# Kernel tuning notes

Measured on AMD Instinct MI355X. Metric: run time of the kernel, lower is better.

## Reference

```python
import jax, jax.numpy as jnp
import numpy as np

N = 100000   # node_num / batch_node_num (full-graph batch, identity remap)
E = 600000   # edges in adj[nodes, :]
D_IN = 128
D_OUT = 128
MASK = (1.0, 1.0, 0.0, 0.0)  # self-loop mask per `ind` in original forward


def setup_inputs() -> dict:
    key = jax.random.key(0)
    ks = jax.random.split(key, 6)
    feat = jax.random.normal(ks[0], (N, D_IN), dtype=jnp.float32)
    edge_src = jax.random.randint(ks[1], (E,), 0, N)
    edge_dst = jax.random.randint(ks[2], (E,), 0, N)
    W_edge = jax.random.uniform(ks[3], (E,), dtype=jnp.float32)  # W[u][v] per edge
    W1 = jax.random.normal(ks[4], (D_IN, D_OUT), dtype=jnp.float32) / np.sqrt(D_IN).astype(np.float32)
    b1 = jnp.zeros((D_OUT,), jnp.float32)
    W2 = jax.random.normal(ks[5], (D_OUT, D_OUT), dtype=jnp.float32) / np.sqrt(D_OUT).astype(np.float32)
    b2 = jnp.zeros((D_OUT,), jnp.float32)
    return {"feat": feat, "W_edge": W_edge, "W1": W1, "b1": b1, "W2": W2,
            "b2": b2, "edge_src": edge_src, "edge_dst": edge_dst, "ind": 2}


def reference(feat, W_edge, W1, b1, W2, b2, edge_src, edge_dst, ind):
    # values: self-loop edges get mask[ind], others 1 (torch.where on edges[:,0]==edges[:,1])
    mask_val = MASK[ind]  # ind is a static Python int
    values = jnp.where(edge_src == edge_dst, jnp.float32(mask_val), jnp.float32(1.0))
    # degree[v] = row-sum of matrix_coo (spmm with ones); temp_e = degree[dst_e]
    degree = jax.ops.segment_sum(values, edge_src, num_segments=N)
    # new_embeddings = Linear -> Tanh -> Linear on features of (all) unique nodes
    h = jnp.tanh(feat @ W1 + b1) @ W2 + b2  # [N, D_OUT]
    # matrix = matrix_neighbor .* matrix_weight -> per-edge weight degree[dst]*W[u][v]
    w = degree[edge_dst] * W_edge  # [E]
    # results = spmm(matrix, new_embeddings); row_sum = spmm(matrix, ones)
    results = jax.ops.segment_sum(w[:, None] * h[edge_dst], edge_src, num_segments=N)
    row_sum = jax.ops.segment_sum(w, edge_src, num_segments=N)
    row_sum = jnp.where(row_sum == 0, jnp.float32(1.0), row_sum)
    return results / row_sum[:, None]
```

## Files before the change

### kernel.cpp

```cpp
#include <hip/hip_runtime.h>


constexpr int D = 128;
constexpr int MAXDEG = 24;
constexpr int OVF_CAP = 131072;

typedef __attribute__((ext_vector_type(8))) short short8;
typedef __attribute__((ext_vector_type(4))) float f32x4;
struct ushort8_s { unsigned short v[8]; };

__device__ __forceinline__ unsigned short f2bf(float x) {
    unsigned int u = __float_as_uint(x);
    u += 0x7fffu + ((u >> 16) & 1u);
    return (unsigned short)(u >> 16);
}
__device__ __forceinline__ float bflo(unsigned int u) { return __uint_as_float(u << 16); }
__device__ __forceinline__ float bfhi(unsigned int u) { return __uint_as_float(u & 0xffff0000u); }
__device__ __forceinline__ float fast_tanh(float x) {
    float e = exp2f(x * 2.885390081777927f);
    return fmaf(-2.0f, __builtin_amdgcn_rcpf(e + 1.0f), 1.0f);
}
__device__ __forceinline__ int swz(int row, int kbyte) {
    return (row * 256 + kbyte) ^ ((row & 7) << 4);
}

__global__ __launch_bounds__(256) void k_init(const float* __restrict__ W1,
                                              const float* __restrict__ W2,
                                              unsigned short* __restrict__ Wt1s,
                                              unsigned short* __restrict__ Wt2s,
                                              int* __restrict__ zbase, int zv4) {
    int b = blockIdx.x;
    if (b < 64) {
        int t = b * 256 + threadIdx.x;
        int k = t >> 7, nn = t & 127;
        int si = swz(nn, k * 2) >> 1;
        Wt1s[si] = f2bf(W1[t]);
        Wt2s[si] = f2bf(W2[t]);
    } else {
        int i = (b - 64) * 256 + threadIdx.x;
        if (i < zv4) ((int4*)zbase)[i] = make_int4(0, 0, 0, 0);
    }
}

__global__ __launch_bounds__(512, 4) void k_mlp_place(
        const float* __restrict__ feat,
        const unsigned short* __restrict__ Wt1s,
        const unsigned short* __restrict__ Wt2s,
        const float* __restrict__ b1, const float* __restrict__ b2,
        unsigned short* __restrict__ hbf, int n,
        const int* __restrict__ src, const int* __restrict__ dst,
        const float* __restrict__ W_edge,
        unsigned int* __restrict__ packed,
        int* __restrict__ ovf_cnt, int4* __restrict__ ovf,
        float2* __restrict__ pairs, int E, int epb) {
    __shared__ unsigned short sW1[128 * D];
    __shared__ unsigned short sW2[128 * D];
    const int t = threadIdx.x;
    const int lane = t & 63;
    const int w = t >> 6;
    const int rl0 = w * 16;
    const int row0 = blockIdx.x * 128 + rl0;
    const int rA = lane & 15;
    const int ks = (lane >> 4) * 8;

    const int ebase = blockIdx.x * epb;
    const int e1 = ebase + t;
    const int e2 = e1 + 512;
    const bool v1 = (t < epb) && (e1 < E);
    const bool v2 = (t < epb - 512) && (e2 < E);
    int s1 = 0, d1 = 0, s2 = 0, d2 = 0;
    float ew1 = 0.f, ew2 = 0.f;
    if (v1) { s1 = src[e1]; d1 = dst[e1]; ew1 = W_edge[e1]; }
    if (v2) { s2 = src[e2]; d2 = dst[e2]; ew2 = W_edge[e2]; }

    float4 f[4][2];
    {
        int gr = row0 + rA;
        bool ok = gr < n;
        const float* fp = &feat[(size_t)(ok ? gr : 0) * D + ks];
#pragma unroll
        for (int kc = 0; kc < 4; ++kc) {
            f[kc][0] = ok ? *(const float4*)(fp + kc * 32) : make_float4(0.f, 0.f, 0.f, 0.f);
            f[kc][1] = ok ? *(const float4*)(fp + kc * 32 + 4) : make_float4(0.f, 0.f, 0.f, 0.f);
        }
    }

    {
        const ushort8_s* g1 = (const ushort8_s*)Wt1s;
        const ushort8_s* g2 = (const ushort8_s*)Wt2s;
        ushort8_s* l1 = (ushort8_s*)sW1;
        ushort8_s* l2 = (ushort8_s*)sW2;
#pragma unroll
        for (int j = 0; j < 4; ++j) {
            int c = t + j * 512;
            l1[c] = g1[c];
            l2[c] = g2[c];
        }
    }

    unsigned int old1 = 0, old2 = 0;
    if (v1) old1 = atomicAdd(&packed[s1], (s1 == d1) ? 0x10001u : 1u);
    if (v2) old2 = atomicAdd(&packed[s2], (s2 == d2) ? 0x10001u : 1u);

    float bias1[8], bias2[8];
#pragma unroll
    for (int nf = 0; nf < 8; ++nf) {
        bias1[nf] = b1[nf * 16 + rA];
        bias2[nf] = b2[nf * 16 + rA];
    }

    short8 afrag[4];
#pragma unroll
    for (int kc = 0; kc < 4; ++kc) {
        float4 f0 = f[kc][0], f1 = f[kc][1];
        short8 a;
        a[0] = (short)f2bf(f0.x); a[1] = (short)f2bf(f0.y);
        a[2] = (short)f2bf(f0.z); a[3] = (short)f2bf(f0.w);
        a[4] = (short)f2bf(f1.x); a[5] = (short)f2bf(f1.y);
        a[6] = (short)f2bf(f1.z); a[7] = (short)f2bf(f1.w);
        afrag[kc] = a;
    }

    __syncthreads();

    f32x4 acc[8];
#pragma unroll
    for (int nf = 0; nf < 8; ++nf) acc[nf] = (f32x4){0.f, 0.f, 0.f, 0.f};

#pragma unroll
    for (int kc = 0; kc < 4; ++kc) {
        const int kb = (kc * 32 + ks) * 2;
#pragma unroll
        for (int nf = 0; nf < 8; ++nf) {
            const int rb = nf * 16 + rA;
            short8 b = *(short8*)((char*)sW1 + swz(rb, kb));
            acc[nf] = __builtin_amdgcn_mfma_f32_16x16x32_bf16(afrag[kc], b, acc[nf], 0, 0, 0);
        }
    }

    __syncthreads();

#pragma unroll
    for (int nf = 0; nf < 8; ++nf) {
        const int col = nf * 16 + rA;
#pragma unroll
        for (int i = 0; i < 4; ++i) {
            const int rl = rl0 + (lane >> 4) * 4 + i;
            unsigned short hv = f2bf(fast_tanh(acc[nf][i] + bias1[nf]));
            *(unsigned short*)((char*)sW1 + swz(rl, col * 2)) = hv;
        }
    }

#pragma unroll
    for (int nf = 0; nf < 8; ++nf) acc[nf] = (f32x4){0.f, 0.f, 0.f, 0.f};

#pragma unroll
    for (int kc = 0; kc < 4; ++kc) {
        const int kb = (kc * 32 + ks) * 2;
        const int ra0 = rl0 + rA;
        short8 a0 = *(short8*)((char*)sW1 + swz(ra0, kb));
#pragma unroll
        for (int nf = 0; nf < 8; ++nf) {
            const int rb = nf * 16 + rA;
            short8 b = *(short8*)((char*)sW2 + swz(rb, kb));
            acc[nf] = __builtin_amdgcn_mfma_f32_16x16x32_bf16(a0, b, acc[nf], 0, 0, 0);
        }
    }

#pragma unroll
    for (int nf = 0; nf < 8; ++nf) {
        const int col = nf * 16 + rA;
#pragma unroll
        for (int i = 0; i < 4; ++i) {
            const int rl = rl0 + (lane >> 4) * 4 + i;
            unsigned short hv = f2bf(acc[nf][i] + bias2[nf]);
            *(unsigned short*)((char*)sW1 + swz(rl, col * 2)) = hv;
        }
    }

    for (int c = lane; c < 256; c += 64) {
        int r = c >> 4, k0 = (c & 15) * 8;
        int gr = row0 + r;
        if (gr < n) {
            int rl = rl0 + r;
            short8 v = *(short8*)((char*)sW1 + swz(rl, k0 * 2));
            *(short8*)&hbf[(size_t)gr * D + k0] = v;
        }
    }

    if (v1) {
        int rank = (int)(old1 & 0xffffu);
        if (rank < MAXDEG) {
            unsigned long long pk =
                (unsigned long long)(unsigned int)d1 |
                ((unsigned long long)__float_as_uint(ew1) << 32);
            __builtin_nontemporal_store(pk, (unsigned long long*)&pairs[(size_t)s1 * MAXDEG + rank]);
        } else {
            int oi = atomicAdd(ovf_cnt, 1);
            if (oi < OVF_CAP) ovf[oi] = make_int4(s1, d1, __float_as_int(ew1), 0);
        }
    }
    if (v2) {
        int rank = (int)(old2 & 0xffffu);
        if (rank < MAXDEG) {
            unsigned long long pk =
                (unsigned long long)(unsigned int)d2 |
                ((unsigned long long)__float_as_uint(ew2) << 32);
            __builtin_nontemporal_store(pk, (unsigned long long*)&pairs[(size_t)s2 * MAXDEG + rank]);
        } else {
            int oi = atomicAdd(ovf_cnt, 1);
            if (oi < OVF_CAP) ovf[oi] = make_int4(s2, d2, __float_as_int(ew2), 0);
        }
    }
}

__global__ __launch_bounds__(256) void k_aggregate(const unsigned int* __restrict__ packed,
                                                   const float2* __restrict__ pairs,
                                                   const int* __restrict__ ovf_cnt,
                                                   const int4* __restrict__ ovf,
                                                   const unsigned short* __restrict__ hbf,
                                                   const int* __restrict__ indp,
                                                   float* __restrict__ out, int n) {
    long long tid = (long long)blockIdx.x * 256 + threadIdx.x;
    int node = (int)(tid >> 4);
    int li = (int)(tid & 15);
    int lane = threadIdx.x & 63;
    if (node >= n) return;
    const float maskm1 = ((indp[0] < 2) ? 1.0f : 0.0f) - 1.0f;

    int cnt = (int)(packed[node] & 0xffffu);
    int mt = (cnt < MAXDEG) ? cnt : MAXDEG;

    float acc[8];
#pragma unroll
    for (int j = 0; j < 8; ++j) acc[j] = 0.f;
    float rsp = 0.f;
    const int gbase = lane & 48;
    const float2* prow = &pairs[(size_t)node * MAXDEG];

    auto fma8 = [&](float w, uint4 h) {
        acc[0] = fmaf(w, bflo(h.x), acc[0]); acc[1] = fmaf(w, bfhi(h.x), acc[1]);
        acc[2] = fmaf(w, bflo(h.y), acc[2]); acc[3] = fmaf(w, bfhi(h.y), acc[3]);
        acc[4] = fmaf(w, bflo(h.z), acc[4]); acc[5] = fmaf(w, bfhi(h.z), acc[5]);
        acc[6] = fmaf(w, bflo(h.w), acc[6]); acc[7] = fmaf(w, bfhi(h.w), acc[7]);
    };

    for (int base = 0; base < mt; base += 16) {
        int mm = mt - base;
        mm = (mm > 16) ? 16 : mm;
        float wv = 0.f;
        float dv = 0.f;
        if (li < mm) {
            float2 p = prow[base + li];
            dv = p.x;
            int d = __float_as_int(p.x);
            unsigned int pkd = packed[d];
            float deg = (float)(pkd & 0xffffu) + maskm1 * (float)(pkd >> 16);
            wv = deg * p.y;
        }
        rsp += wv;
        int i = 0;
        for (; i + 3 < mm; i += 4) {
            int d0 = __float_as_int(__shfl(dv, gbase + i));
            float w0 = __shfl(wv, gbase + i);
            int d1 = __float_as_int(__shfl(dv, gbase + i + 1));
            float w1 = __shfl(wv, gbase + i + 1);
            int d2 = __float_as_int(__shfl(dv, gbase + i + 2));
            float w2 = __shfl(wv, gbase + i + 2);
            int d3 = __float_as_int(__shfl(dv, gbase + i + 3));
            float w3 = __shfl(wv, gbase + i + 3);
            uint4 h0 = *(const uint4*)&hbf[(size_t)d0 * D + li * 8];
            uint4 h1 = *(const uint4*)&hbf[(size_t)d1 * D + li * 8];
            uint4 h2 = *(const uint4*)&hbf[(size_t)d2 * D + li * 8];
            uint4 h3 = *(const uint4*)&hbf[(size_t)d3 * D + li * 8];
            fma8(w0, h0); fma8(w1, h1); fma8(w2, h2); fma8(w3, h3);
        }
        for (; i + 1 < mm; i += 2) {
            int d0 = __float_as_int(__shfl(dv, gbase + i));
            float w0 = __shfl(wv, gbase + i);
            int d1 = __float_as_int(__shfl(dv, gbase + i + 1));
            float w1 = __shfl(wv, gbase + i + 1);
            uint4 h0 = *(const uint4*)&hbf[(size_t)d0 * D + li * 8];
            uint4 h1 = *(const uint4*)&hbf[(size_t)d1 * D + li * 8];
            fma8(w0, h0); fma8(w1, h1);
        }
        if (i < mm) {
            int d0 = __float_as_int(__shfl(dv, gbase + i));
            float w0 = __shfl(wv, gbase + i);
            uint4 h0 = *(const uint4*)&hbf[(size_t)d0 * D + li * 8];
            fma8(w0, h0);
        }
    }

    int ovn = *ovf_cnt;
    if (ovn > OVF_CAP) ovn = OVF_CAP;
    for (int i = 0; i < ovn; ++i) {
        int4 tq = ovf[i];
        if (tq.x == node) {
            int d = tq.y;
            unsigned int pkd = packed[d];
            float deg = (float)(pkd & 0xffffu) + maskm1 * (float)(pkd >> 16);
            float w = deg * __int_as_float(tq.z);
            if (li == 0) rsp += w;
            uint4 h = *(const uint4*)&hbf[(size_t)d * D + li * 8];
            fma8(w, h);
        }
    }

    rsp += __shfl_xor(rsp, 1);
    rsp += __shfl_xor(rsp, 2);
    rsp += __shfl_xor(rsp, 4);
    rsp += __shfl_xor(rsp, 8);
    rsp = (rsp == 0.f) ? 1.f : rsp;
    float inv = 1.0f / rsp;
    float4 o0, o1;
    o0.x = acc[0] * inv; o0.y = acc[1] * inv; o0.z = acc[2] * inv; o0.w = acc[3] * inv;
    o1.x = acc[4] * inv; o1.y = acc[5] * inv; o1.z = acc[6] * inv; o1.w = acc[7] * inv;
    float* op = &out[(size_t)node * D + li * 8];
    *(float4*)op = o0;
    *(float4*)(op + 4) = o1;
}

extern "C" void kernel_launch(void* const* d_in, const int* in_sizes, int n_in,
                              void* d_out, int out_size, void* d_ws, size_t ws_size,
                              hipStream_t stream) {
    const float* feat   = (const float*)d_in[0];
    const float* W_edge = (const float*)d_in[1];
    const float* W1     = (const float*)d_in[2];
    const float* b1     = (const float*)d_in[3];
    const float* W2     = (const float*)d_in[4];
    const float* b2     = (const float*)d_in[5];
    const int* edge_src = (const int*)d_in[6];
    const int* edge_dst = (const int*)d_in[7];
    const int* indp     = (const int*)d_in[8];

    const int n = in_sizes[0] / D;
    const int E = in_sizes[6];

    char* ws = (char*)d_ws;
    unsigned short* Wt1s = (unsigned short*)ws;
    unsigned short* Wt2s = Wt1s + D * D;
    unsigned int* packed = (unsigned int*)(Wt2s + D * D);
    int* ovf_cnt         = (int*)(packed + n);
    int4* ovf            = (int4*)((char*)ovf_cnt + 16);
    float2* pairs        = (float2*)(ovf + OVF_CAP);
    unsigned short* hbf  = (unsigned short*)(pairs + (size_t)n * MAXDEG);

    const int zbytes = n * 4 + 16;
    const int zv4 = zbytes / 16;
    const int zb = (zv4 + 255) / 256;
    k_init<<<64 + zb, 256, 0, stream>>>(W1, W2, Wt1s, Wt2s, (int*)packed, zv4);

    const int nm = (n + 127) / 128;
    const int epb = (E + nm - 1) / nm;
    k_mlp_place<<<nm, 512, 0, stream>>>(feat, Wt1s, Wt2s, b1, b2, hbf, n,
                                        edge_src, edge_dst, W_edge,
                                        packed, ovf_cnt, ovf, pairs, E, epb);

    long long athreads = (long long)n * 16;
    k_aggregate<<<(int)((athreads + 255) / 256), 256, 0, stream>>>(packed, pairs, ovf_cnt,
                                                                   ovf, hbf, indp,
                                                                   (float*)d_out, n);
}
```

Measured before the change: 98.47 us.

## Read second-layer weights from global memory instead of LDS, halving shared memory

The second MLP weight matrix is no longer staged into shared memory. It is stored transposed and unswizzled in global memory, and the B fragments are read directly from there (L1/L2 cached) during the second MFMA loop. This halves LDS use per block (64KB to 32KB), which could allow more resident blocks per CU and removes the W2 copy. The edge placement stores also switch from nontemporal to plain float2 stores, which changes how those writes interact with the cache before the aggregate kernel reads them. The cost is global-memory latency on the B-fragment loads inside the MFMA loop.

```diff
diff --git a/kernel.cpp b/kernel.cpp
--- a/kernel.cpp
+++ b/kernel.cpp
@@ -27,15 +27,14 @@
 __global__ __launch_bounds__(256) void k_init(const float* __restrict__ W1,
                                               const float* __restrict__ W2,
                                               unsigned short* __restrict__ Wt1s,
-                                              unsigned short* __restrict__ Wt2s,
+                                              unsigned short* __restrict__ Wt2t,
                                               int* __restrict__ zbase, int zv4) {
     int b = blockIdx.x;
     if (b < 64) {
         int t = b * 256 + threadIdx.x;
         int k = t >> 7, nn = t & 127;
-        int si = swz(nn, k * 2) >> 1;
-        Wt1s[si] = f2bf(W1[t]);
-        Wt2s[si] = f2bf(W2[t]);
+        Wt1s[swz(nn, k * 2) >> 1] = f2bf(W1[t]);
+        Wt2t[nn * D + k] = f2bf(W2[t]);
     } else {
         int i = (b - 64) * 256 + threadIdx.x;
         if (i < zv4) ((int4*)zbase)[i] = make_int4(0, 0, 0, 0);
@@ -45,7 +44,7 @@
 __global__ __launch_bounds__(512, 4) void k_mlp_place(
         const float* __restrict__ feat,
         const unsigned short* __restrict__ Wt1s,
-        const unsigned short* __restrict__ Wt2s,
+        const unsigned short* __restrict__ Wt2t,
         const float* __restrict__ b1, const float* __restrict__ b2,
         unsigned short* __restrict__ hbf, int n,
         const int* __restrict__ src, const int* __restrict__ dst,
@@ -54,7 +53,6 @@
         int* __restrict__ ovf_cnt, int4* __restrict__ ovf,
         float2* __restrict__ pairs, int E, int epb) {
     __shared__ unsigned short sW1[128 * D];
-    __shared__ unsigned short sW2[128 * D];
     const int t = threadIdx.x;
     const int lane = t & 63;
     const int w = t >> 6;
@@ -87,14 +85,11 @@
 
     {
         const ushort8_s* g1 = (const ushort8_s*)Wt1s;
-        const ushort8_s* g2 = (const ushort8_s*)Wt2s;
         ushort8_s* l1 = (ushort8_s*)sW1;
-        ushort8_s* l2 = (ushort8_s*)sW2;
 #pragma unroll
         for (int j = 0; j < 4; ++j) {
             int c = t + j * 512;
             l1[c] = g1[c];
-            l2[c] = g2[c];
         }
     }
 
@@ -161,8 +156,7 @@
         short8 a0 = *(short8*)((char*)sW1 + swz(ra0, kb));
 #pragma unroll
         for (int nf = 0; nf < 8; ++nf) {
-            const int rb = nf * 16 + rA;
-            short8 b = *(short8*)((char*)sW2 + swz(rb, kb));
+            short8 b = *(const short8*)&Wt2t[(nf * 16 + rA) * D + kc * 32 + ks];
             acc[nf] = __builtin_amdgcn_mfma_f32_16x16x32_bf16(a0, b, acc[nf], 0, 0, 0);
         }
     }
@@ -191,10 +185,10 @@
     if (v1) {
         int rank = (int)(old1 & 0xffffu);
         if (rank < MAXDEG) {
-            unsigned long long pk =
-                (unsigned long long)(unsigned int)d1 |
-                ((unsigned long long)__float_as_uint(ew1) << 32);
-            __builtin_nontemporal_store(pk, (unsigned long long*)&pairs[(size_t)s1 * MAXDEG + rank]);
+            float2 p;
+            p.x = __int_as_float(d1);
+            p.y = ew1;
+            pairs[(size_t)s1 * MAXDEG + rank] = p;
         } else {
             int oi = atomicAdd(ovf_cnt, 1);
             if (oi < OVF_CAP) ovf[oi] = make_int4(s1, d1, __float_as_int(ew1), 0);
@@ -203,10 +197,10 @@
     if (v2) {
         int rank = (int)(old2 & 0xffffu);
         if (rank < MAXDEG) {
-            unsigned long long pk =
-                (unsigned long long)(unsigned int)d2 |
-                ((unsigned long long)__float_as_uint(ew2) << 32);
-            __builtin_nontemporal_store(pk, (unsigned long long*)&pairs[(size_t)s2 * MAXDEG + rank]);
+            float2 p;
+            p.x = __int_as_float(d2);
+            p.y = ew2;
+            pairs[(size_t)s2 * MAXDEG + rank] = p;
         } else {
             int oi = atomicAdd(ovf_cnt, 1);
             if (oi < OVF_CAP) ovf[oi] = make_int4(s2, d2, __float_as_int(ew2), 0);
@@ -339,8 +333,8 @@
 
     char* ws = (char*)d_ws;
     unsigned short* Wt1s = (unsigned short*)ws;
-    unsigned short* Wt2s = Wt1s + D * D;
-    unsigned int* packed = (unsigned int*)(Wt2s + D * D);
+    unsigned short* Wt2t = Wt1s + D * D;
+    unsigned int* packed = (unsigned int*)(Wt2t + D * D);
     int* ovf_cnt         = (int*)(packed + n);
     int4* ovf            = (int4*)((char*)ovf_cnt + 16);
     float2* pairs        = (float2*)(ovf + OVF_CAP);
@@ -349,11 +343,11 @@
     const int zbytes = n * 4 + 16;
     const int zv4 = zbytes / 16;
     const int zb = (zv4 + 255) / 256;
-    k_init<<<64 + zb, 256, 0, stream>>>(W1, W2, Wt1s, Wt2s, (int*)packed, zv4);
+    k_init<<<64 + zb, 256, 0, stream>>>(W1, W2, Wt1s, Wt2t, (int*)packed, zv4);
 
     const int nm = (n + 127) / 128;
     const int epb = (E + nm - 1) / nm;
-    k_mlp_place<<<nm, 512, 0, stream>>>(feat, Wt1s, Wt2s, b1, b2, hbf, n,
+    k_mlp_place<<<nm, 512, 0, stream>>>(feat, Wt1s, Wt2t, b1, b2, hbf, n,
                                         edge_src, edge_dst, W_edge,
                                         packed, ovf_cnt, ovf, pairs, E, epb);
 
```

After: 114.2 us. 1.16x slower.
